# Performance work log

Hardware: AMD Instinct MI355X
Metric: run time of the kernel (lower is better)

## Reference

```python
import jax, jax.numpy as jnp
import numpy as np

B, N, H, G, WIN, MH = 8, 8192, 128, 16, 3, 16
EPS = 1e-8


def _edges(n, w):
    # local sequence edges: i -> j for j in [i-w, i+w], j != i, 0 <= j < n
    i = np.arange(n)
    off = np.concatenate([np.arange(-w, 0), np.arange(1, w + 1)])
    j = i[:, None] + off[None, :]
    m = (j >= 0) & (j < n)
    src = np.broadcast_to(i[:, None], j.shape)[m]
    dst = j[m]
    return jnp.asarray(src, jnp.int32), jnp.asarray(dst, jnp.int32)


def setup_inputs() -> dict:
    key = jax.random.key(0)
    ks = jax.random.split(key, 10)
    d = {}
    d['x_scalar'] = jax.random.normal(ks[0], (B, N, H), jnp.float32)
    d['vec'] = jax.random.normal(ks[1], (B, N, 3, H), jnp.float32)
    d['W_geom'] = jax.random.normal(ks[2], (H, G), jnp.float32) / np.sqrt(H).astype(np.float32)
    d['q_w1'] = jax.random.normal(ks[3], (2, MH), jnp.float32) * 0.5
    d['q_b1'] = jnp.zeros((MH,), jnp.float32)
    d['q_w2'] = jax.random.normal(ks[4], (MH, 1), jnp.float32) * 0.25
    d['q_b2'] = jnp.zeros((1,), jnp.float32)
    d['k_w1'] = jax.random.normal(ks[5], (2, MH), jnp.float32) * 0.5
    d['k_b1'] = jnp.zeros((MH,), jnp.float32)
    d['k_w2'] = jax.random.normal(ks[6], (MH, 1), jnp.float32) * 0.25
    d['k_b2'] = jnp.zeros((1,), jnp.float32)
    d['Wq'] = jax.random.normal(ks[7], (G, H), jnp.float32) / np.sqrt(G).astype(np.float32)
    d['bq'] = jnp.zeros((H,), jnp.float32)
    d['Wk'] = jax.random.normal(ks[8], (G, H), jnp.float32) / np.sqrt(G).astype(np.float32)
    d['bk'] = jnp.zeros((H,), jnp.float32)
    return d


def _mlp(f, w1, b1, w2, b2):
    # f: (B,E,G,2) -> (B,E,G)
    return (jax.nn.silu(f @ w1 + b1) @ w2 + b2)[..., 0]


def reference(x_scalar, vec, W_geom, q_w1, q_b1, q_w2, q_b2,
              k_w1, k_b1, k_w2, k_b2, Wq, bq, Wk, bk):
    b, n, h = x_scalar.shape
    src, dst = _edges(n, WIN)
    # project vectors into geometry subspace: (B,N,3,G)
    vec_geom = jnp.einsum('bnch,hg->bncg', vec, W_geom)
    v_i = vec_geom[:, src]          # (B,E,3,G)
    v_j = vec_geom[:, dst]
    b_ij = v_j - v_i
    norm_b = jnp.maximum(jnp.linalg.norm(b_ij, axis=2, keepdims=True), EPS)
    e_ij = b_ij / norm_b            # unit edge directions (B,E,3,G)
    # scatter-add edge directions back to source nodes: (B,N,3,G)
    u = jnp.zeros((b, n, 3, G), x_scalar.dtype).at[:, src].add(e_ij)
    u_i = u[:, src]
    u_j = u[:, dst]
    dot_ui_e = (u_i * e_ij).sum(axis=2)                       # (B,E,G)
    norm_ui = jnp.maximum(jnp.linalg.norm(u_i, axis=2), EPS)
    ang_ij = jnp.clip(dot_ui_e / norm_ui, -1.0, 1.0)
    u_i_perp = u_i - dot_ui_e[:, :, None, :] * e_ij
    dot_uj_e = (u_j * e_ij).sum(axis=2)
    u_j_perp = u_j - dot_uj_e[:, :, None, :] * e_ij
    dot_perp = (u_i_perp * u_j_perp).sum(axis=2)
    np_i = jnp.maximum(jnp.linalg.norm(u_i_perp, axis=2), EPS)
    np_j = jnp.maximum(jnp.linalg.norm(u_j_perp, axis=2), EPS)
    dih_cos = jnp.clip(dot_perp / jnp.maximum(np_i * np_j, EPS), -1.0, 1.0)
    feats = jnp.stack([ang_ij, dih_cos], axis=-1)             # (B,E,G,2)
    g_geom_q = _mlp(feats, q_w1, q_b1, q_w2, q_b2)            # (B,E,G)
    g_geom_k = _mlp(feats, k_w1, k_b1, k_w2, k_b2)
    g_q = jax.nn.sigmoid(g_geom_q @ Wq + bq)                  # (B,E,H)
    g_k = jax.nn.sigmoid(g_geom_k @ Wk + bk)
    s_j = x_scalar[:, dst]                                    # (B,E,H)
    q = jnp.zeros_like(x_scalar).at[:, src].add(g_q * s_j)
    k = jnp.zeros_like(x_scalar).at[:, src].add(g_k * s_j)
    return q, k
```

## Files before the change

### kernel.cpp

```cpp
#include <hip/hip_runtime.h>

constexpr int NB = 8;
constexpr int NN = 8192;
constexpr int NH = 128;
constexpr int NG = 16;
constexpr int NT = 36;
constexpr int NT1 = NT + 1;
constexpr float NLOG2E = -1.44269504088896f;

typedef short s16x8 __attribute__((ext_vector_type(8)));
typedef float f32x4 __attribute__((ext_vector_type(4)));

__device__ __forceinline__ float frcp(float x) { return __builtin_amdgcn_rcpf(x); }
__device__ __forceinline__ float frsq(float x) { return __builtin_amdgcn_rsqf(x); }
__device__ __forceinline__ float fexp2(float x) {
#if __has_builtin(__builtin_amdgcn_exp2f)
    return __builtin_amdgcn_exp2f(x);
#else
    return __expf(x * 0.69314718056f);
#endif
}
__device__ __forceinline__ float fsigmoid(float x) { return frcp(1.f + __expf(-x)); }
__device__ __forceinline__ float fsilu(float x) { return x * fsigmoid(x); }
__device__ __forceinline__ float fclamp1(float x) { return fminf(fmaxf(x, -1.f), 1.f); }

__device__ __forceinline__ unsigned short f2bf(float x) {
    unsigned u = __builtin_bit_cast(unsigned, x);
    return (unsigned short)((u + 0x7FFFu + ((u >> 16) & 1u)) >> 16);
}
__device__ __forceinline__ unsigned packh2(float a, float b) {
    unsigned short lo = __builtin_bit_cast(unsigned short, (__fp16)a);
    unsigned short hi = __builtin_bit_cast(unsigned short, (__fp16)b);
    return (unsigned)lo | ((unsigned)hi << 16);
}
__device__ __forceinline__ float h2lo(unsigned u) {
    return (float)__builtin_bit_cast(__fp16, (unsigned short)(u & 0xFFFFu));
}
__device__ __forceinline__ float h2hi(unsigned u) {
    return (float)__builtin_bit_cast(__fp16, (unsigned short)(u >> 16));
}

__global__ __launch_bounds__(256) void k_table(
    const float* __restrict__ qw1, const float* __restrict__ qb1,
    const float* __restrict__ qw2, const float* __restrict__ qb2,
    const float* __restrict__ kw1, const float* __restrict__ kb1,
    const float* __restrict__ kw2, const float* __restrict__ kb2,
    unsigned* __restrict__ T) {
    int idx = blockIdx.x * 256 + threadIdx.x;
    if (idx >= NT1 * NT1) return;
    int ia = idx / NT1, id = idx % NT1;
    float a = -1.f + (float)ia * (2.f / NT);
    float d = -1.f + (float)id * (2.f / NT);
    float fq = qb2[0], fk = kb2[0];
#pragma unroll
    for (int m = 0; m < 16; ++m) {
        float hq = fmaf(a, qw1[m], fmaf(d, qw1[16 + m], qb1[m]));
        float hk = fmaf(a, kw1[m], fmaf(d, kw1[16 + m], kb1[m]));
        fq = fmaf(fsilu(hq), qw2[m], fq);
        fk = fmaf(fsilu(hk), kw2[m], fk);
    }
    T[idx] = packh2(fq, fk);
}

__global__ __launch_bounds__(256) void k_prep(
    const float* __restrict__ Wq, const float* __restrict__ bq,
    const float* __restrict__ Wk, const float* __restrict__ bk,
    s16x8* __restrict__ WB, float* __restrict__ BB) {
    int tid = threadIdx.x;
    for (int slot = tid; slot < 2 * 8 * 32; slot += 256) {
        int lane_in = slot & 31;
        int frag = slot >> 5;
        int fqk = frag >> 3, fht = frag & 7;
        const float* W = fqk ? Wk : Wq;
        int k0 = (lane_in >> 4) * 8, fcol = lane_in & 15;
        s16x8 v;
#pragma unroll
        for (int i = 0; i < 8; ++i)
            v[i] = (short)f2bf(NLOG2E * W[(k0 + i) * NH + fht * 16 + fcol]);
        WB[slot] = v;
    }
    if (tid < NH) BB[tid] = NLOG2E * bq[tid];
    else BB[tid] = NLOG2E * bk[tid - NH];
}

__global__ __launch_bounds__(256) void k_vecgeom(const float* __restrict__ vec,
                                                 const float* __restrict__ Wg,
                                                 float* __restrict__ vg) {
    __shared__ float Wl[NH * NG];
    for (int t = threadIdx.x; t < NH * NG; t += 256) Wl[t] = Wg[t];
    __syncthreads();

    int idx = blockIdx.x * 256 + threadIdx.x;
    int gq = idx & 3;
    int rc = idx >> 2;
    const float4* vrow = reinterpret_cast<const float4*>(vec + rc * NH);
    float a0 = 0.f, a1 = 0.f, a2 = 0.f, a3 = 0.f;
#pragma unroll 8
    for (int h4 = 0; h4 < 32; ++h4) {
        float4 v = vrow[h4];
        int h = h4 * 4;
        float4 w0 = *reinterpret_cast<const float4*>(&Wl[(h + 0) * NG + gq * 4]);
        float4 w1 = *reinterpret_cast<const float4*>(&Wl[(h + 1) * NG + gq * 4]);
        float4 w2 = *reinterpret_cast<const float4*>(&Wl[(h + 2) * NG + gq * 4]);
        float4 w3 = *reinterpret_cast<const float4*>(&Wl[(h + 3) * NG + gq * 4]);
        a0 = fmaf(v.x, w0.x, a0); a1 = fmaf(v.x, w0.y, a1); a2 = fmaf(v.x, w0.z, a2); a3 = fmaf(v.x, w0.w, a3);
        a0 = fmaf(v.y, w1.x, a0); a1 = fmaf(v.y, w1.y, a1); a2 = fmaf(v.y, w1.z, a2); a3 = fmaf(v.y, w1.w, a3);
        a0 = fmaf(v.z, w2.x, a0); a1 = fmaf(v.z, w2.y, a1); a2 = fmaf(v.z, w2.z, a2); a3 = fmaf(v.z, w2.w, a3);
        a0 = fmaf(v.w, w3.x, a0); a1 = fmaf(v.w, w3.y, a1); a2 = fmaf(v.w, w3.z, a2); a3 = fmaf(v.w, w3.w, a3);
    }
    *reinterpret_cast<float4*>(vg + rc * NG + gq * 4) = make_float4(a0, a1, a2, a3);
}

__global__ __launch_bounds__(256) void k_u(const float* __restrict__ vg,
                                           float* __restrict__ u) {
    int idx = blockIdx.x * 256 + threadIdx.x;
    int g = idx & 15;
    int bn = idx >> 4;
    int n = bn & (NN - 1);
    int base_i = bn * 48 + g;
    float vi0 = vg[base_i], vi1 = vg[base_i + 16], vi2 = vg[base_i + 32];
    float a0 = 0.f, a1 = 0.f, a2 = 0.f;
#pragma unroll
    for (int e = 0; e < 6; ++e) {
        int off = (e < 3) ? (e - 3) : (e - 2);
        int j = n + off;
        if (j < 0 || j >= NN) continue;
        int base_j = base_i + off * 48;
        float d0 = vg[base_j] - vi0;
        float d1 = vg[base_j + 16] - vi1;
        float d2 = vg[base_j + 32] - vi2;
        float r = frsq(fmaxf(d0 * d0 + d1 * d1 + d2 * d2, 1e-16f));
        a0 = fmaf(d0, r, a0); a1 = fmaf(d1, r, a1); a2 = fmaf(d2, r, a2);
    }
    u[base_i] = a0; u[base_i + 16] = a1; u[base_i + 32] = a2;
}

__device__ __forceinline__ void edge_gates(
    int base_i, int base_j,
    float vi0, float vi1, float vi2,
    float ui0, float ui1, float ui2, float rnui,
    const float* __restrict__ vg, const float* __restrict__ u,
    const unsigned (&Ts)[NT1 * NT1], float& fq, float& fk) {
    float d0 = vg[base_j] - vi0;
    float d1 = vg[base_j + 16] - vi1;
    float d2 = vg[base_j + 32] - vi2;
    float rb = frsq(fmaxf(d0 * d0 + d1 * d1 + d2 * d2, 1e-16f));
    float e0 = d0 * rb, e1 = d1 * rb, e2 = d2 * rb;
    float uj0 = u[base_j], uj1 = u[base_j + 16], uj2 = u[base_j + 32];
    float die = ui0 * e0 + ui1 * e1 + ui2 * e2;
    float ang = fclamp1(die * rnui);
    float p0 = ui0 - die * e0, p1 = ui1 - die * e1, p2 = ui2 - die * e2;
    float dje = uj0 * e0 + uj1 * e1 + uj2 * e2;
    float q0 = uj0 - dje * e0, q1 = uj1 - dje * e1, q2 = uj2 - dje * e2;
    float dp = p0 * q0 + p1 * q1 + p2 * q2;
    float pp = fmaxf(p0 * p0 + p1 * p1 + p2 * p2, 1e-16f);
    float qq = fmaxf(q0 * q0 + q1 * q1 + q2 * q2, 1e-16f);
    float dih = fclamp1(dp * frsq(pp * qq));

    float af = fmaf(ang, (float)NT * 0.5f, (float)NT * 0.5f);
    float df_ = fmaf(dih, (float)NT * 0.5f, (float)NT * 0.5f);
    int ia = min((int)af, NT - 1);
    int id = min((int)df_, NT - 1);
    float fa = af - (float)ia;
    float fd = df_ - (float)id;
    const unsigned* t0 = &Ts[ia * NT1 + id];
    unsigned c00 = t0[0], c01 = t0[1], c10 = t0[NT1], c11 = t0[NT1 + 1];
    float l0q = fmaf(fd, h2lo(c01) - h2lo(c00), h2lo(c00));
    float h0q = fmaf(fd, h2lo(c11) - h2lo(c10), h2lo(c10));
    fq = fmaf(fa, h0q - l0q, l0q);
    float l0k = fmaf(fd, h2hi(c01) - h2hi(c00), h2hi(c00));
    float h0k = fmaf(fd, h2hi(c11) - h2hi(c10), h2hi(c10));
    fk = fmaf(fa, h0k - l0k, l0k);
}

template <bool INT>
__device__ __forceinline__ void phaseA(
    int bn0, int n0, int w, int lane,
    const float* __restrict__ vg, const float* __restrict__ u,
    const unsigned (&Ts)[NT1 * NT1],
    unsigned short (&As)[2][6][16][16]) {
    int nl = lane >> 4, g = lane & 15;
    int node = w * 4 + nl;
    int bn = bn0 + node;
    int base_i = bn * 48 + g;
    float vi0 = vg[base_i], vi1 = vg[base_i + 16], vi2 = vg[base_i + 32];
    float ui0 = u[base_i],  ui1 = u[base_i + 16],  ui2 = u[base_i + 32];
    float rnui = frsq(fmaxf(ui0 * ui0 + ui1 * ui1 + ui2 * ui2, 1e-16f));
#pragma unroll
    for (int e = 0; e < 6; ++e) {
        int off = (e < 3) ? (e - 3) : (e - 2);
        bool valid = INT || ((unsigned)(n0 + node + off) < (unsigned)NN);
        float fq = 0.f, fk = 0.f;
        if (valid)
            edge_gates(base_i, base_i + off * 48, vi0, vi1, vi2,
                       ui0, ui1, ui2, rnui, vg, u, Ts, fq, fk);
        As[0][e][node][g] = f2bf(fq);
        As[1][e][node][g] = f2bf(fk);
    }
}

template <bool INT>
__device__ __forceinline__ void phaseB(
    int bn0, int n0, int qk, int hh, int lane,
    const float* __restrict__ xs,
    const unsigned short (&As)[2][6][16][16],
    const s16x8 (&Wl)[2][8][32], const float (&bs)[2][NH],
    float* __restrict__ out) {
    int c = lane & 15, rg = lane >> 4;

    s16x8 afr[6];
    int aidx = c * 2 + rg;
#pragma unroll
    for (int e = 0; e < 6; ++e)
        afr[e] = (lane < 32)
            ? reinterpret_cast<const s16x8*>(&As[qk][e][0][0])[aidx]
            : (s16x8)0;

#pragma unroll
    for (int t = 0; t < 4; ++t) {
        int ht = hh * 4 + t;
        float xr[10];
#pragma unroll
        for (int d = 0; d < 10; ++d) {
            if (INT) {
                xr[d] = xs[(size_t)(bn0 + rg * 4 + d - 3) * NH + ht * 16 + c];
            } else {
                int gidx = bn0 + rg * 4 + d - 3;
                gidx = min(max(gidx, 0), NB * NN - 1);
                xr[d] = xs[(size_t)gidx * NH + ht * 16 + c];
            }
        }
        s16x8 bfr = (lane < 32) ? Wl[qk][ht][lane] : (s16x8)0;
        float b = bs[qk][ht * 16 + c];
        f32x4 bias4 = {b, b, b, b};
        f32x4 acc = {0.f, 0.f, 0.f, 0.f};
#pragma unroll
        for (int e = 0; e < 6; ++e) {
            f32x4 cc = __builtin_amdgcn_mfma_f32_16x16x32_bf16(afr[e], bfr, bias4, 0, 0, 0);
            int off = (e < 3) ? (e - 3) : (e - 2);
#pragma unroll
            for (int r = 0; r < 4; ++r) {
                float pr = frcp(1.f + fexp2(cc[r]));
                if (!INT) {
                    int jn = n0 + rg * 4 + r + off;
                    pr = ((unsigned)jn < (unsigned)NN) ? pr : 0.f;
                }
                acc[r] = fmaf(pr, xr[r + off + 3], acc[r]);
            }
        }
        float* o = out + (size_t)(bn0 + rg * 4) * NH + ht * 16 + c;
#pragma unroll
        for (int r = 0; r < 4; ++r) o[r * NH] = acc[r];
    }
}

__global__ __launch_bounds__(256, 4) void k_main(
    const float* __restrict__ vg, const float* __restrict__ u,
    const float* __restrict__ xs, const unsigned* __restrict__ T,
    const s16x8* __restrict__ WB, const float* __restrict__ BB,
    float* __restrict__ outq, float* __restrict__ outk) {
    __shared__ unsigned Ts[NT1 * NT1];
    __shared__ __align__(16) unsigned short As[2][6][16][16];
    __shared__ s16x8 Wl[2][8][32];
    __shared__ float bs[2][NH];

    int tid = threadIdx.x;
    for (int t = tid; t < NT1 * NT1; t += 256) Ts[t] = T[t];
    {
        s16x8* wl = &Wl[0][0][0];
        for (int slot = tid; slot < 2 * 8 * 32; slot += 256) wl[slot] = WB[slot];
        if (tid < 2 * NH) (&bs[0][0])[tid] = BB[tid];
    }

    int w = tid >> 6, lane = tid & 63;
    int qk = w >> 1, hh = w & 1;

    __syncthreads();

#pragma unroll
    for (int it = 0; it < 4; ++it) {
        int grp = blockIdx.x * 4 + it;
        int bn0 = grp * 16;
        int n0 = bn0 & (NN - 1);
        bool interior = (n0 != 0) && (n0 != NN - 16);

        if (interior) phaseA<true>(bn0, n0, w, lane, vg, u, Ts, As);
        else          phaseA<false>(bn0, n0, w, lane, vg, u, Ts, As);

        __syncthreads();

        float* out = qk ? outk : outq;
        if (interior) phaseB<true>(bn0, n0, qk, hh, lane, xs, As, Wl, bs, out);
        else          phaseB<false>(bn0, n0, qk, hh, lane, xs, As, Wl, bs, out);

        __syncthreads();
    }
}

extern "C" void kernel_launch(void* const* d_in, const int* in_sizes, int n_in,
                              void* d_out, int out_size, void* d_ws, size_t ws_size,
                              hipStream_t stream) {
    const float* xs   = (const float*)d_in[0];
    const float* vec  = (const float*)d_in[1];
    const float* Wg   = (const float*)d_in[2];
    const float* qw1  = (const float*)d_in[3];
    const float* qb1  = (const float*)d_in[4];
    const float* qw2  = (const float*)d_in[5];
    const float* qb2  = (const float*)d_in[6];
    const float* kw1  = (const float*)d_in[7];
    const float* kb1  = (const float*)d_in[8];
    const float* kw2  = (const float*)d_in[9];
    const float* kb2  = (const float*)d_in[10];
    const float* Wq   = (const float*)d_in[11];
    const float* bq   = (const float*)d_in[12];
    const float* Wk   = (const float*)d_in[13];
    const float* bk   = (const float*)d_in[14];

    size_t vg_f = (size_t)NB * NN * 48;
    float* vg = (float*)d_ws;
    float* u  = vg + vg_f;
    unsigned* T = (unsigned*)(u + vg_f);
    s16x8* WB = (s16x8*)((char*)(T + NT1 * NT1) + (16 - ((NT1 * NT1 * 4) & 15)) % 16
                          + ((uintptr_t)(T + NT1 * NT1) & 15 ? 0 : 0));
    WB = (s16x8*)(((uintptr_t)(T + NT1 * NT1) + 15) & ~(uintptr_t)15);
    float* BB = (float*)(WB + 2 * 8 * 32);
    float* outq = (float*)d_out;
    float* outk = outq + (size_t)NB * NN * NH;

    k_table<<<dim3((NT1 * NT1 + 255) / 256), dim3(256), 0, stream>>>(
        qw1, qb1, qw2, qb2, kw1, kb1, kw2, kb2, T);
    k_prep<<<dim3(1), dim3(256), 0, stream>>>(Wq, bq, Wk, bk, WB, BB);
    k_vecgeom<<<dim3(3072), dim3(256), 0, stream>>>(vec, Wg, vg);
    k_u<<<dim3(4096), dim3(256), 0, stream>>>(vg, u);
    k_main<<<dim3(1024), dim3(256), 0, stream>>>(
        vg, u, xs, T, WB, BB, outq, outk);
}
```

Before: 83.94 us.

## Shrink gate lookup table and split main kernel into one-group 128-thread blocks

The main kernel moves from 256-thread blocks that loop over four 16-node groups to 128-thread blocks that each handle one group, launched as four times as many blocks. Each wave now does two nodes' worth of phase A and all eight H tiles of one of q or k in phase B, which runs at raised wave priority. MFMA weights and biases are read straight from global memory instead of being staged in LDS. The interpolation table resolution drops from 36 to 24 bins, which cuts table staging cost but coarsens the MLP approximation and may change accuracy.

```diff
diff --git a/kernel.cpp b/kernel.cpp
--- a/kernel.cpp
+++ b/kernel.cpp
@@ -4,7 +4,7 @@
 constexpr int NN = 8192;
 constexpr int NH = 128;
 constexpr int NG = 16;
-constexpr int NT = 36;
+constexpr int NT = 24;
 constexpr int NT1 = NT + 1;
 constexpr float NLOG2E = -1.44269504088896f;
 
@@ -175,36 +175,39 @@
 
 template <bool INT>
 __device__ __forceinline__ void phaseA(
-    int bn0, int n0, int w, int lane,
+    int bn0, int n0, int sub, int lane,
     const float* __restrict__ vg, const float* __restrict__ u,
     const unsigned (&Ts)[NT1 * NT1],
     unsigned short (&As)[2][6][16][16]) {
     int nl = lane >> 4, g = lane & 15;
-    int node = w * 4 + nl;
-    int bn = bn0 + node;
-    int base_i = bn * 48 + g;
-    float vi0 = vg[base_i], vi1 = vg[base_i + 16], vi2 = vg[base_i + 32];
-    float ui0 = u[base_i],  ui1 = u[base_i + 16],  ui2 = u[base_i + 32];
-    float rnui = frsq(fmaxf(ui0 * ui0 + ui1 * ui1 + ui2 * ui2, 1e-16f));
-#pragma unroll
-    for (int e = 0; e < 6; ++e) {
-        int off = (e < 3) ? (e - 3) : (e - 2);
-        bool valid = INT || ((unsigned)(n0 + node + off) < (unsigned)NN);
-        float fq = 0.f, fk = 0.f;
-        if (valid)
-            edge_gates(base_i, base_i + off * 48, vi0, vi1, vi2,
-                       ui0, ui1, ui2, rnui, vg, u, Ts, fq, fk);
-        As[0][e][node][g] = f2bf(fq);
-        As[1][e][node][g] = f2bf(fk);
+#pragma unroll
+    for (int i = 0; i < 2; ++i) {
+        int node = sub * 8 + i * 4 + nl;
+        int bn = bn0 + node;
+        int base_i = bn * 48 + g;
+        float vi0 = vg[base_i], vi1 = vg[base_i + 16], vi2 = vg[base_i + 32];
+        float ui0 = u[base_i],  ui1 = u[base_i + 16],  ui2 = u[base_i + 32];
+        float rnui = frsq(fmaxf(ui0 * ui0 + ui1 * ui1 + ui2 * ui2, 1e-16f));
+#pragma unroll
+        for (int e = 0; e < 6; ++e) {
+            int off = (e < 3) ? (e - 3) : (e - 2);
+            bool valid = INT || ((unsigned)(n0 + node + off) < (unsigned)NN);
+            float fq = 0.f, fk = 0.f;
+            if (valid)
+                edge_gates(base_i, base_i + off * 48, vi0, vi1, vi2,
+                           ui0, ui1, ui2, rnui, vg, u, Ts, fq, fk);
+            As[0][e][node][g] = f2bf(fq);
+            As[1][e][node][g] = f2bf(fk);
+        }
     }
 }
 
 template <bool INT>
 __device__ __forceinline__ void phaseB(
-    int bn0, int n0, int qk, int hh, int lane,
+    int bn0, int n0, int qk, int lane,
     const float* __restrict__ xs,
     const unsigned short (&As)[2][6][16][16],
-    const s16x8 (&Wl)[2][8][32], const float (&bs)[2][NH],
+    const s16x8* __restrict__ WB, const float* __restrict__ BB,
     float* __restrict__ out) {
     int c = lane & 15, rg = lane >> 4;
 
@@ -216,9 +219,9 @@
             ? reinterpret_cast<const s16x8*>(&As[qk][e][0][0])[aidx]
             : (s16x8)0;
 
-#pragma unroll
-    for (int t = 0; t < 4; ++t) {
-        int ht = hh * 4 + t;
+    __builtin_amdgcn_s_setprio(1);
+#pragma unroll
+    for (int ht = 0; ht < 8; ++ht) {
         float xr[10];
 #pragma unroll
         for (int d = 0; d < 10; ++d) {
@@ -230,8 +233,8 @@
                 xr[d] = xs[(size_t)gidx * NH + ht * 16 + c];
             }
         }
-        s16x8 bfr = (lane < 32) ? Wl[qk][ht][lane] : (s16x8)0;
-        float b = bs[qk][ht * 16 + c];
+        s16x8 bfr = (lane < 32) ? WB[(qk * 8 + ht) * 32 + lane] : (s16x8)0;
+        float b = BB[qk * NH + ht * 16 + c];
         f32x4 bias4 = {b, b, b, b};
         f32x4 acc = {0.f, 0.f, 0.f, 0.f};
 #pragma unroll
@@ -252,49 +255,36 @@
 #pragma unroll
         for (int r = 0; r < 4; ++r) o[r * NH] = acc[r];
     }
-}
-
-__global__ __launch_bounds__(256, 4) void k_main(
+    __builtin_amdgcn_s_setprio(0);
+}
+
+__global__ __launch_bounds__(128, 4) void k_main(
     const float* __restrict__ vg, const float* __restrict__ u,
     const float* __restrict__ xs, const unsigned* __restrict__ T,
     const s16x8* __restrict__ WB, const float* __restrict__ BB,
     float* __restrict__ outq, float* __restrict__ outk) {
     __shared__ unsigned Ts[NT1 * NT1];
     __shared__ __align__(16) unsigned short As[2][6][16][16];
-    __shared__ s16x8 Wl[2][8][32];
-    __shared__ float bs[2][NH];
 
     int tid = threadIdx.x;
-    for (int t = tid; t < NT1 * NT1; t += 256) Ts[t] = T[t];
-    {
-        s16x8* wl = &Wl[0][0][0];
-        for (int slot = tid; slot < 2 * 8 * 32; slot += 256) wl[slot] = WB[slot];
-        if (tid < 2 * NH) (&bs[0][0])[tid] = BB[tid];
-    }
-
-    int w = tid >> 6, lane = tid & 63;
-    int qk = w >> 1, hh = w & 1;
+    for (int t = tid; t < NT1 * NT1; t += 128) Ts[t] = T[t];
+
+    int sub = tid >> 6, lane = tid & 63;
+    int grp = blockIdx.x;
+    int bn0 = grp * 16;
+    int n0 = bn0 & (NN - 1);
+    bool interior = (n0 != 0) && (n0 != NN - 16);
 
     __syncthreads();
 
-#pragma unroll
-    for (int it = 0; it < 4; ++it) {
-        int grp = blockIdx.x * 4 + it;
-        int bn0 = grp * 16;
-        int n0 = bn0 & (NN - 1);
-        bool interior = (n0 != 0) && (n0 != NN - 16);
-
-        if (interior) phaseA<true>(bn0, n0, w, lane, vg, u, Ts, As);
-        else          phaseA<false>(bn0, n0, w, lane, vg, u, Ts, As);
-
-        __syncthreads();
-
-        float* out = qk ? outk : outq;
-        if (interior) phaseB<true>(bn0, n0, qk, hh, lane, xs, As, Wl, bs, out);
-        else          phaseB<false>(bn0, n0, qk, hh, lane, xs, As, Wl, bs, out);
-
-        __syncthreads();
-    }
+    if (interior) phaseA<true>(bn0, n0, sub, lane, vg, u, Ts, As);
+    else          phaseA<false>(bn0, n0, sub, lane, vg, u, Ts, As);
+
+    __syncthreads();
+
+    float* out = sub ? outk : outq;
+    if (interior) phaseB<true>(bn0, n0, sub, lane, xs, As, WB, BB, out);
+    else          phaseB<false>(bn0, n0, sub, lane, xs, As, WB, BB, out);
 }
 
 extern "C" void kernel_launch(void* const* d_in, const int* in_sizes, int n_in,
@@ -320,9 +310,7 @@
     float* vg = (float*)d_ws;
     float* u  = vg + vg_f;
     unsigned* T = (unsigned*)(u + vg_f);
-    s16x8* WB = (s16x8*)((char*)(T + NT1 * NT1) + (16 - ((NT1 * NT1 * 4) & 15)) % 16
-                          + ((uintptr_t)(T + NT1 * NT1) & 15 ? 0 : 0));
-    WB = (s16x8*)(((uintptr_t)(T + NT1 * NT1) + 15) & ~(uintptr_t)15);
+    s16x8* WB = (s16x8*)(((uintptr_t)(T + NT1 * NT1) + 15) & ~(uintptr_t)15);
     float* BB = (float*)(WB + 2 * 8 * 32);
     float* outq = (float*)d_out;
     float* outk = outq + (size_t)NB * NN * NH;
@@ -332,6 +320,6 @@
     k_prep<<<dim3(1), dim3(256), 0, stream>>>(Wq, bq, Wk, bk, WB, BB);
     k_vecgeom<<<dim3(3072), dim3(256), 0, stream>>>(vec, Wg, vg);
     k_u<<<dim3(4096), dim3(256), 0, stream>>>(vg, u);
-    k_main<<<dim3(1024), dim3(256), 0, stream>>>(
+    k_main<<<dim3(4096), dim3(128), 0, stream>>>(
         vg, u, xs, T, WB, BB, outq, outk);
 }
```

New measurement: 83.61 us. Within noise of the previous version (-0.4%).
